# Performance work log

Measured on AMD Instinct MI355X. Metric: run time of the kernel, lower is better.

Reference implementation:

```python
import jax, jax.numpy as jnp
import numpy as np

B, N, D, H, HD, HID, RP_HID = 4, 512, 1024, 16, 64, 4096, 64
EPS = 1e-5


def _ln(h, g, b):
    mu = h.mean(-1, keepdims=True)
    var = h.var(-1, keepdims=True)
    return (h - mu) / jnp.sqrt(var + EPS) * g + b


def setup_inputs() -> dict:
    key = jax.random.key(0)
    ks = jax.random.split(key, 24)
    s = 0.05
    return {
        "x": jax.random.normal(ks[0], (B, N, D), jnp.float32),
        "t_emb": jax.random.normal(ks[1], (B, D), jnp.float32),
        "rel_pos_matrix": jax.random.normal(ks[2], (B, N, N, 2), jnp.float32),
        "agent_mask": jax.random.randint(ks[3], (B, N), 0, 2).astype(jnp.int32),
        # adaLN modulation: Linear(D, 6D)
        "w_ada": jax.random.normal(ks[4], (6 * D, D), jnp.float32) * s,
        "b_ada": jnp.zeros((6 * D,), jnp.float32),
        # LayerNorms
        "g1": jnp.ones((D,), jnp.float32),
        "beta1": jnp.zeros((D,), jnp.float32),
        "g2": jnp.ones((D,), jnp.float32),
        "beta2": jnp.zeros((D,), jnp.float32),
        # attention qkv / proj
        "w_qkv": jax.random.normal(ks[5], (3 * D, D), jnp.float32) * s,
        "b_qkv": jnp.zeros((3 * D,), jnp.float32),
        "w_proj": jax.random.normal(ks[6], (D, D), jnp.float32) * s,
        "b_proj": jnp.zeros((D,), jnp.float32),
        # rel-pos bias MLP: Linear(2,64) -> ReLU -> Linear(64,H)
        "w_rp1": jax.random.normal(ks[7], (RP_HID, 2), jnp.float32) * s,
        "b_rp1": jnp.zeros((RP_HID,), jnp.float32),
        "w_rp2": jax.random.normal(ks[8], (H, RP_HID), jnp.float32) * s,
        "b_rp2": jnp.zeros((H,), jnp.float32),
        # MLP: Linear(D, HID) -> GELU -> Linear(HID, D)
        "w_fc1": jax.random.normal(ks[9], (HID, D), jnp.float32) * s,
        "b_fc1": jnp.zeros((HID,), jnp.float32),
        "w_fc2": jax.random.normal(ks[10], (D, HID), jnp.float32) * s,
        "b_fc2": jnp.zeros((D,), jnp.float32),
    }


def reference(x, t_emb, rel_pos_matrix, agent_mask,
              w_ada, b_ada, g1, beta1, w_qkv, b_qkv, w_proj, b_proj,
              w_rp1, b_rp1, w_rp2, b_rp2, g2, beta2,
              w_fc1, b_fc1, w_fc2, b_fc2):
    b, n, d = x.shape
    # adaLN: SiLU -> Linear -> 6 chunks of [B, D]
    mod = jax.nn.silu(t_emb) @ w_ada.T + b_ada
    shift_s, scale_s, gate_s, shift_m, scale_m, gate_m = jnp.split(mod, 6, axis=1)

    # ---- spatial attention branch ----
    xn = _ln(x, g1, beta1) * (1.0 + scale_s[:, None, :]) + shift_s[:, None, :]
    qkv = (xn @ w_qkv.T + b_qkv).reshape(b, n, 3, H, HD)
    q, k, v = jnp.moveaxis(qkv, 2, 0)  # each [B, N, H, HD]
    attn = jnp.einsum('bnhd,bmhd->bhnm', q, k) * (HD ** -0.5)
    # relative-position bias MLP: [B,N,N,2] -> [B,N,N,H] -> [B,H,N,N]
    bias = jax.nn.relu(rel_pos_matrix @ w_rp1.T + b_rp1) @ w_rp2.T + b_rp2
    attn = attn + bias.transpose(0, 3, 1, 2)
    mask = agent_mask.astype(bool)[:, None, None, :]  # key-side mask [B,1,1,N]
    attn = jnp.where(mask, attn, -jnp.inf)
    p = jax.nn.softmax(attn, axis=-1)
    out = jnp.einsum('bhnm,bmhd->bnhd', p, v).reshape(b, n, d)
    out = out @ w_proj.T + b_proj
    x = x + gate_s[:, None, :] * out

    # ---- gated MLP branch ----
    xn = _ln(x, g2, beta2) * (1.0 + scale_m[:, None, :]) + shift_m[:, None, :]
    h = jax.nn.gelu(xn @ w_fc1.T + b_fc1, approximate=False)
    x = x + gate_m[:, None, :] * (h @ w_fc2.T + b_fc2)
    return x
```

## Files before the change

kernel.cpp:

```cpp
#include <hip/hip_runtime.h>


#define B_ 4
#define N_ 512
#define D_ 1024
#define H_ 16
#define HID_ 4096
#define M_ (B_*N_)

typedef unsigned short u16;
typedef __attribute__((ext_vector_type(8))) short bf16x8;
typedef __attribute__((ext_vector_type(4))) float f32x4;

__device__ __forceinline__ float b2f(u16 u){
  union { unsigned int i; float f; } x; x.i = ((unsigned int)u) << 16; return x.f;
}
__device__ __forceinline__ u16 f2b(float f){
  unsigned int u = __float_as_uint(f);
  return (u16)((u + 0x7fffu + ((u >> 16) & 1u)) >> 16);
}

__device__ __forceinline__ void gload16(const u16* __restrict__ g, u16* l){
#if defined(__has_builtin) && __has_builtin(__builtin_amdgcn_global_load_lds)
  __builtin_amdgcn_global_load_lds(
      (const __attribute__((address_space(1))) unsigned int*)g,
      (__attribute__((address_space(3))) unsigned int*)l, 16, 0, 0);
#else
  *(uint4*)l = *(const uint4*)g;
#endif
}

__global__ __launch_bounds__(256) void k_cvt2(const float* __restrict__ sA, u16* __restrict__ dA,
    int nA, const float* __restrict__ sB, u16* __restrict__ dB){
  int blk = blockIdx.x;
  const float* s; u16* d; size_t i;
  if (blk < nA){ s = sA; d = dA; i = ((size_t)blk*256 + threadIdx.x)*8; }
  else { s = sB; d = dB; i = ((size_t)(blk-nA)*256 + threadIdx.x)*8; }
  float4 a = *(const float4*)(s+i), b = *(const float4*)(s+i+4);
  u16 o[8] = {f2b(a.x),f2b(a.y),f2b(a.z),f2b(a.w),f2b(b.x),f2b(b.y),f2b(b.z),f2b(b.w)};
  *(uint4*)(d+i) = *(const uint4*)o;
}

__global__ __launch_bounds__(256) void k_mod(const float* __restrict__ t_emb,
    const float* __restrict__ w_ada, const float* __restrict__ b_ada,
    float* __restrict__ mod)
{
  __shared__ float st[D_];
  int b = blockIdx.y;
  for (int i = threadIdx.x; i < D_; i += 256){
    float x = t_emb[b*D_ + i];
    st[i] = x / (1.f + __expf(-x));
  }
  __syncthreads();
  int j = blockIdx.x * 256 + threadIdx.x;
  const float* wr = w_ada + (size_t)j * D_;
  float acc = b_ada[j];
  for (int k = 0; k < D_; k += 8){
    float4 p0 = *(const float4*)(wr + k);
    float4 p1 = *(const float4*)(wr + k + 4);
    acc += p0.x*st[k+0] + p0.y*st[k+1] + p0.z*st[k+2] + p0.w*st[k+3];
    acc += p1.x*st[k+4] + p1.y*st[k+5] + p1.z*st[k+6] + p1.w*st[k+7];
  }
  mod[b*6*D_ + j] = acc;
}

__global__ __launch_bounds__(256) void k_lnmod(const float* __restrict__ xin,
    const float* __restrict__ g, const float* __restrict__ be,
    const float* __restrict__ mod, int shift_idx, int scale_idx,
    u16* __restrict__ xn)
{
  int row = blockIdx.x;
  int b = row >> 9;
  float v[4]; float s = 0.f, s2 = 0.f;
  #pragma unroll
  for (int i=0;i<4;i++){
    float x = xin[(size_t)row*D_ + threadIdx.x + i*256];
    v[i] = x; s += x; s2 += x*x;
  }
  #pragma unroll
  for (int o=32;o>0;o>>=1){ s += __shfl_down(s,o); s2 += __shfl_down(s2,o); }
  __shared__ float rs[4], rs2[4];
  int w = threadIdx.x >> 6;
  if ((threadIdx.x & 63)==0){ rs[w]=s; rs2[w]=s2; }
  __syncthreads();
  s = rs[0]+rs[1]+rs[2]+rs[3]; s2 = rs2[0]+rs2[1]+rs2[2]+rs2[3];
  float mu = s * (1.f/D_);
  float var = s2 * (1.f/D_) - mu*mu;
  float rstd = rsqrtf(var + 1e-5f);
  const float* mrow = mod + b*6*D_;
  #pragma unroll
  for (int i=0;i<4;i++){
    int d = threadIdx.x + i*256;
    float xg = (v[i]-mu)*rstd*g[d] + be[d];
    xn[(size_t)row*D_ + d] = f2b(xg * (1.f + mrow[scale_idx*D_ + d]) + mrow[shift_idx*D_ + d]);
  }
}

__global__ __launch_bounds__(256) void k_bias(const float* __restrict__ rel,
    const int* __restrict__ amask,
    const float* __restrict__ w_rp1, const float* __restrict__ b_rp1,
    const float* __restrict__ w_rp2, const float* __restrict__ b_rp2,
    u16* __restrict__ biasbuf)
{
  __shared__ __align__(16) u16 Hs[256*72];
  __shared__ __align__(16) u16 Bs[16*272];
  __shared__ __align__(16) u16 w2s[16*72];
  __shared__ float b2s[16];
  __shared__ u16 msk[256];
  int mh = blockIdx.x, n = blockIdx.y, b = blockIdx.z;
  int tid = threadIdx.x;
  int w = tid >> 6, lane = tid & 63, ln = lane & 15, quad = lane >> 4;

  for (int i = tid; i < 1024; i += 256) w2s[(i>>6)*72 + (i&63)] = f2b(w_rp2[i]);
  if (tid < 16) b2s[tid] = b_rp2[tid];
  msk[tid] = (u16)(amask[b*N_ + mh*256 + tid] != 0);

  {
    float2 r01 = *(const float2*)(rel + ((size_t)((b*N_ + n)*N_) + mh*256 + tid)*2);
    const float* w1 = w_rp1;
    u16 hv[64];
    #pragma unroll
    for (int j=0;j<64;j++){
      float t = w1[2*j]*r01.x + w1[2*j+1]*r01.y + b_rp1[j];
      hv[j] = f2b(t > 0.f ? t : 0.f);
    }
    uint4* dst = (uint4*)&Hs[tid*72];
    #pragma unroll
    for (int c=0;c<8;c++) dst[c] = *(const uint4*)&hv[c*8];
  }
  __syncthreads();

  bf16x8 af0 = *(const bf16x8*)&w2s[ln*72 + quad*8];
  bf16x8 af1 = *(const bf16x8*)&w2s[ln*72 + 32 + quad*8];

  #pragma unroll
  for (int t=0; t<4; t++){
    int mt = w*4 + t;
    bf16x8 bf0 = *(const bf16x8*)&Hs[(mt*16+ln)*72 + quad*8];
    bf16x8 bf1 = *(const bf16x8*)&Hs[(mt*16+ln)*72 + 32 + quad*8];
    f32x4 c = {};
    c = __builtin_amdgcn_mfma_f32_16x16x32_bf16(af0, bf0, c, 0,0,0);
    c = __builtin_amdgcn_mfma_f32_16x16x32_bf16(af1, bf1, c, 0,0,0);
    bool valid = msk[mt*16 + ln] != 0;
    #pragma unroll
    for (int i=0;i<4;i++){
      int h = quad*4 + i;
      float val = valid ? (c[i] + b2s[h]) : -1e30f;
      Bs[h*272 + mt*16 + ln] = f2b(val);
    }
  }
  __syncthreads();

  #pragma unroll
  for (int it=0; it<8; it++){
    int idx = it*256 + tid;
    int r = idx >> 7, cc = idx & 127;
    size_t rb = (((size_t)(b*H_ + r)*N_) + n)*N_ + mh*256;
    ((unsigned int*)(biasbuf + rb))[cc] = ((const unsigned int*)(Bs + r*272))[cc];
  }
}

enum { EPI_FC1=0, EPI_PART=1 };

template<int EPI>
__global__ __launch_bounds__(256) void k_gemm(const u16* __restrict__ A,
    const u16* __restrict__ W, const float* __restrict__ Wb, int K, int Kslice,
    int ldc, u16* __restrict__ part01, u16* __restrict__ part23)
{
  __shared__ __align__(16) u16 Al[128*64];
  __shared__ __align__(16) u16 Wl[128*64];
  int row0 = blockIdx.y*128, col0 = blockIdx.x*128;
  int tid = threadIdx.x;
  int w = tid >> 6, lane = tid & 63, ln = lane & 15, quad = lane >> 4;
  int wy = w >> 1, wx = w & 1;
  int srow = tid >> 3;
  int schunk = (tid & 7) ^ (srow & 7);
  const u16* Ag = A + (size_t)(row0 + srow)*K + schunk*8;
  const u16* Wg = W + (size_t)(col0 + srow)*K + schunk*8;
  int aoff[4][2], woff[4][2];
  #pragma unroll
  for (int ms=0; ms<4; ms++){
    int r = 64*wy + 16*ms + ln;
    #pragma unroll
    for (int kk=0; kk<2; kk++)
      aoff[ms][kk] = r*64 + (((kk*4+quad) ^ (ln&7))*8);
  }
  #pragma unroll
  for (int ns=0; ns<4; ns++){
    int r = 64*wx + 16*ns + ln;
    #pragma unroll
    for (int kk=0; kk<2; kk++)
      woff[ns][kk] = r*64 + (((kk*4+quad) ^ (ln&7))*8);
  }
  f32x4 acc[4][4] = {};
  int kbeg = blockIdx.z * Kslice;
  for (int k0 = kbeg; k0 < kbeg + Kslice; k0 += 64){
    #pragma unroll
    for (int i=0;i<4;i++){
      gload16(Ag + k0 + (size_t)(32*i)*K, Al + i*2048 + tid*8);
      gload16(Wg + k0 + (size_t)(32*i)*K, Wl + i*2048 + tid*8);
    }
    __syncthreads();
    #pragma unroll
    for (int kk=0; kk<2; kk++){
      bf16x8 af[4], bfr[4];
      #pragma unroll
      for (int ms=0; ms<4; ms++) af[ms]  = *(const bf16x8*)&Al[aoff[ms][kk]];
      #pragma unroll
      for (int ns=0; ns<4; ns++) bfr[ns] = *(const bf16x8*)&Wl[woff[ns][kk]];
      #pragma unroll
      for (int ms=0; ms<4; ms++)
        #pragma unroll
        for (int ns=0; ns<4; ns++)
          acc[ms][ns] = __builtin_amdgcn_mfma_f32_16x16x32_bf16(af[ms], bfr[ns], acc[ms][ns], 0,0,0);
    }
    __syncthreads();
  }

  u16* pbase = (EPI == EPI_PART)
             ? ((blockIdx.z < 2 ? part01 : part23) + (size_t)(blockIdx.z & 1)*M_*ldc)
             : part01;
  #pragma unroll
  for (int ms=0; ms<4; ms++){
    #pragma unroll
    for (int ns=0; ns<4; ns++){
      int c = col0 + 64*wx + 16*ns + ln;
      float wb = (EPI == EPI_FC1) ? Wb[c] : 0.f;
      #pragma unroll
      for (int i=0;i<4;i++){
        int r = row0 + 64*wy + 16*ms + quad*4 + i;
        float val = acc[ms][ns][i] + wb;
        if (EPI == EPI_FC1){
          float gl = 0.5f*val*(1.f + erff(val*0.70710678f));
          pbase[(size_t)r*ldc + c] = f2b(gl);
        } else {
          pbase[(size_t)r*ldc + c] = f2b(val);
        }
      }
    }
  }
}

__global__ __launch_bounds__(256) void k_redq(const u16* __restrict__ part,
    const float* __restrict__ Wb, u16* __restrict__ qkvb)
{
  size_t i = ((size_t)blockIdx.x*256 + threadIdx.x)*4;
  int c = (int)(i % 3072);
  uint2 p0 = *(const uint2*)(part + i);
  uint2 p1 = *(const uint2*)(part + (size_t)M_*3072 + i);
  float4 bi = *(const float4*)(Wb + c);
  u16 o[4];
  o[0] = f2b(b2f((u16)(p0.x & 0xffff)) + b2f((u16)(p1.x & 0xffff)) + bi.x);
  o[1] = f2b(b2f((u16)(p0.x >> 16))    + b2f((u16)(p1.x >> 16))    + bi.y);
  o[2] = f2b(b2f((u16)(p0.y & 0xffff)) + b2f((u16)(p1.y & 0xffff)) + bi.z);
  o[3] = f2b(b2f((u16)(p0.y >> 16))    + b2f((u16)(p1.y >> 16))    + bi.w);
  *(uint2*)(qkvb + i) = *(const uint2*)o;
}

template<int GIDX>
__global__ __launch_bounds__(256) void k_red4(const u16* __restrict__ p01,
    const u16* __restrict__ p23, const float* __restrict__ Wb,
    const float* __restrict__ mod, const float* __restrict__ resid,
    float* __restrict__ outp)
{
  size_t i = ((size_t)blockIdx.x*256 + threadIdx.x)*4;
  int c = (int)(i & 1023); int r = (int)(i >> 10); int b = r >> 9;
  uint2 a0 = *(const uint2*)(p01 + i);
  uint2 a1 = *(const uint2*)(p01 + (size_t)M_*D_ + i);
  uint2 a2 = *(const uint2*)(p23 + i);
  uint2 a3 = *(const uint2*)(p23 + (size_t)M_*D_ + i);
  float4 pv;
  pv.x = b2f((u16)(a0.x&0xffff)) + b2f((u16)(a1.x&0xffff)) + b2f((u16)(a2.x&0xffff)) + b2f((u16)(a3.x&0xffff));
  pv.y = b2f((u16)(a0.x>>16))    + b2f((u16)(a1.x>>16))    + b2f((u16)(a2.x>>16))    + b2f((u16)(a3.x>>16));
  pv.z = b2f((u16)(a0.y&0xffff)) + b2f((u16)(a1.y&0xffff)) + b2f((u16)(a2.y&0xffff)) + b2f((u16)(a3.y&0xffff));
  pv.w = b2f((u16)(a0.y>>16))    + b2f((u16)(a1.y>>16))    + b2f((u16)(a2.y>>16))    + b2f((u16)(a3.y>>16));
  float4 x4 = *(const float4*)(resid + i);
  float4 bi = *(const float4*)(Wb + c);
  float4 g4 = *(const float4*)(mod + b*6*D_ + GIDX*D_ + c);
  float4 o;
  o.x = x4.x + g4.x*(pv.x + bi.x);
  o.y = x4.y + g4.y*(pv.y + bi.y);
  o.z = x4.z + g4.z*(pv.z + bi.z);
  o.w = x4.w + g4.w*(pv.w + bi.w);
  *(float4*)(outp + i) = o;
}

__global__ __launch_bounds__(256) void k_attn(const u16* __restrict__ qkv,
    const u16* __restrict__ biasbuf, u16* __restrict__ attn_out)
{
  __shared__ __align__(16) u16 Qs[64*72];
  __shared__ __align__(16) u16 Ks[64*72];
  __shared__ __align__(16) u16 Vt[64*72];
  __shared__ __align__(16) u16 Ps[4*16*72];
  int nt = blockIdx.x, h = blockIdx.y, b = blockIdx.z;
  int n0 = nt*64;
  int tid = threadIdx.x;
  int w = tid >> 6, lane = tid & 63, ln = lane & 15, quad = lane >> 4;

  {
    int row = tid >> 2, cb = (tid & 3)*16;
    const u16* src = qkv + (size_t)(b*N_ + n0 + row)*3072 + h*64 + cb;
    uint4 q0 = *(const uint4*)src, q1 = *(const uint4*)(src+8);
    uint4* dst = (uint4*)&Qs[row*72 + cb];
    dst[0] = q0; dst[1] = q1;
  }
  __syncthreads();
  bf16x8 qf[2];
  qf[0] = *(const bf16x8*)&Qs[(16*w+ln)*72 + quad*8];
  qf[1] = *(const bf16x8*)&Qs[(16*w+ln)*72 + 32 + quad*8];

  f32x4 oacc[4] = {};
  float rmax[4] = {-3e38f,-3e38f,-3e38f,-3e38f};
  float rsum[4] = {0.f,0.f,0.f,0.f};
  const u16* bp = biasbuf + (((size_t)(b*H_ + h)*N_) + n0 + 16*w)*N_ + ln;

  for (int mt = 0; mt < 8; mt++){
    __syncthreads();
    {
      int r = tid >> 2, cb = (tid & 3)*16;
      const u16* kp = qkv + (size_t)(b*N_ + mt*64 + r)*3072 + 1024 + h*64 + cb;
      uint4 k0 = *(const uint4*)kp, k1 = *(const uint4*)(kp+8);
      uint4* kd = (uint4*)&Ks[r*72 + cb];
      kd[0] = k0; kd[1] = k1;
      const u16* vp = qkv + (size_t)(b*N_ + mt*64 + r)*3072 + 2048 + h*64 + cb;
      uint4 v0 = *(const uint4*)vp, v1 = *(const uint4*)(vp+8);
      u16 ve[16];
      *(uint4*)&ve[0] = v0; *(uint4*)&ve[8] = v1;
      #pragma unroll
      for (int j=0;j<16;j++) Vt[(cb+j)*72 + r] = ve[j];
    }
    __syncthreads();

    u16 bl[4][4];
    #pragma unroll
    for (int cs=0; cs<4; cs++)
      #pragma unroll
      for (int i=0;i<4;i++)
        bl[cs][i] = bp[(size_t)(quad*4+i)*N_ + mt*64 + 16*cs];

    f32x4 s[4];
    #pragma unroll
    for (int cs=0; cs<4; cs++){
      bf16x8 k0f = *(const bf16x8*)&Ks[(16*cs+ln)*72 + quad*8];
      bf16x8 k1f = *(const bf16x8*)&Ks[(16*cs+ln)*72 + 32 + quad*8];
      f32x4 z = {};
      z = __builtin_amdgcn_mfma_f32_16x16x32_bf16(qf[0], k0f, z, 0,0,0);
      z = __builtin_amdgcn_mfma_f32_16x16x32_bf16(qf[1], k1f, z, 0,0,0);
      s[cs] = z;
    }
    #pragma unroll
    for (int cs=0; cs<4; cs++)
      #pragma unroll
      for (int i=0;i<4;i++)
        s[cs][i] = s[cs][i]*0.125f + b2f(bl[cs][i]);

    #pragma unroll
    for (int i=0;i<4;i++){
      float tm = fmaxf(fmaxf(s[0][i], s[1][i]), fmaxf(s[2][i], s[3][i]));
      #pragma unroll
      for (int o=1;o<16;o<<=1) tm = fmaxf(tm, __shfl_xor(tm, o));
      float nm = fmaxf(rmax[i], tm);
      float alpha = __expf(rmax[i] - nm);
      rmax[i] = nm;
      float ps = 0.f;
      #pragma unroll
      for (int cs=0; cs<4; cs++){
        float p = __expf(s[cs][i] - nm);
        s[cs][i] = p; ps += p;
      }
      #pragma unroll
      for (int o=1;o<16;o<<=1) ps += __shfl_xor(ps, o);
      rsum[i] = rsum[i]*alpha + ps;
      #pragma unroll
      for (int ds=0; ds<4; ds++) oacc[ds][i] *= alpha;
    }

    #pragma unroll
    for (int cs=0; cs<4; cs++)
      #pragma unroll
      for (int i=0;i<4;i++)
        Ps[w*1152 + (quad*4+i)*72 + 16*cs + ln] = f2b(s[cs][i]);

    bf16x8 pf0 = *(const bf16x8*)&Ps[w*1152 + ln*72 + quad*8];
    bf16x8 pf1 = *(const bf16x8*)&Ps[w*1152 + ln*72 + 32 + quad*8];
    #pragma unroll
    for (int ds=0; ds<4; ds++){
      bf16x8 v0f = *(const bf16x8*)&Vt[(16*ds+ln)*72 + quad*8];
      bf16x8 v1f = *(const bf16x8*)&Vt[(16*ds+ln)*72 + 32 + quad*8];
      oacc[ds] = __builtin_amdgcn_mfma_f32_16x16x32_bf16(pf0, v0f, oacc[ds], 0,0,0);
      oacc[ds] = __builtin_amdgcn_mfma_f32_16x16x32_bf16(pf1, v1f, oacc[ds], 0,0,0);
    }
  }

  #pragma unroll
  for (int i=0;i<4;i++){
    float inv = 1.f / rsum[i];
    int r = b*N_ + n0 + 16*w + quad*4 + i;
    #pragma unroll
    for (int ds=0; ds<4; ds++)
      attn_out[(size_t)r*D_ + h*64 + 16*ds + ln] = f2b(oacc[ds][i]*inv);
  }
}

extern "C" void kernel_launch(void* const* d_in, const int* in_sizes, int n_in,
                              void* d_out, int out_size, void* d_ws, size_t ws_size,
                              hipStream_t stream) {
  const float* x      = (const float*)d_in[0];
  const float* t_emb  = (const float*)d_in[1];
  const float* rel    = (const float*)d_in[2];
  const int*   amask  = (const int*)d_in[3];
  const float* w_ada  = (const float*)d_in[4];
  const float* b_ada  = (const float*)d_in[5];
  const float* g1     = (const float*)d_in[6];
  const float* beta1  = (const float*)d_in[7];
  const float* g2     = (const float*)d_in[8];
  const float* beta2  = (const float*)d_in[9];
  const float* w_qkv  = (const float*)d_in[10];
  const float* b_qkv  = (const float*)d_in[11];
  const float* w_proj = (const float*)d_in[12];
  const float* b_proj = (const float*)d_in[13];
  const float* w_rp1  = (const float*)d_in[14];
  const float* b_rp1  = (const float*)d_in[15];
  const float* w_rp2  = (const float*)d_in[16];
  const float* b_rp2  = (const float*)d_in[17];
  const float* w_fc1  = (const float*)d_in[18];
  const float* b_fc1  = (const float*)d_in[19];
  const float* w_fc2  = (const float*)d_in[20];
  const float* b_fc2  = (const float*)d_in[21];
  float* outp = (float*)d_out;

  const size_t MB = 1u<<20;
  char* wsb = (char*)d_ws;
  float* mod   = (float*)(wsb);
  u16*  xn     = (u16*) (wsb + 131072);
  float* xm    = (float*)(wsb + 131072 + 4*MB);
  u16*  wqkvb  = (u16*) (wsb + 131072 + 12*MB);
  u16*  wprojb = (u16*) (wsb + 131072 + 18*MB);
  u16*  partb  = (u16*) (wsb + 131072 + 20*MB);
  char*  S     = wsb + 131072 + 28*MB;
  u16*  qkvb   = (u16*)(S);
  u16*  qkvpart= (u16*)(S + 12*MB);
  u16*  biasb  = (u16*)(S + 12*MB);
  u16*  projp23= (u16*)(S);
  u16*  hb     = (u16*)(S);
  u16*  wfc1b  = (u16*)(S + 16*MB);
  u16*  wfc2b  = (u16*)(S + 24*MB);
  u16*  fc2p23 = (u16*)(S + 32*MB);

  k_cvt2<<<2048, 256, 0, stream>>>(w_qkv, wqkvb, 1536, w_proj, wprojb);
  k_mod<<<dim3(6*D_/256, B_), 256, 0, stream>>>(t_emb, w_ada, b_ada, mod);
  k_lnmod<<<M_, 256, 0, stream>>>(x, g1, beta1, mod, 0, 1, xn);
  k_gemm<EPI_PART><<<dim3(3072/128, M_/128, 2), 256, 0, stream>>>(
      xn, wqkvb, nullptr, D_, D_/2, 3072, qkvpart, qkvpart);
  k_redq<<<6144, 256, 0, stream>>>(qkvpart, b_qkv, qkvb);
  k_bias<<<dim3(2, N_, B_), 256, 0, stream>>>(rel, amask, w_rp1, b_rp1, w_rp2, b_rp2, biasb);
  k_attn<<<dim3(8, H_, B_), 256, 0, stream>>>(qkvb, biasb, xn);
  k_cvt2<<<4096, 256, 0, stream>>>(w_fc1, wfc1b, 2048, w_fc2, wfc2b);
  k_gemm<EPI_PART><<<dim3(D_/128, M_/128, 4), 256, 0, stream>>>(
      xn, wprojb, nullptr, D_, D_/4, D_, partb, projp23);
  k_red4<2><<<2048, 256, 0, stream>>>(partb, projp23, b_proj, mod, x, xm);
  k_lnmod<<<M_, 256, 0, stream>>>(xm, g2, beta2, mod, 3, 4, xn);
  k_gemm<EPI_FC1><<<dim3(HID_/128, M_/128), 256, 0, stream>>>(
      xn, wfc1b, b_fc1, D_, D_, HID_, hb, nullptr);
  k_gemm<EPI_PART><<<dim3(D_/128, M_/128, 4), 256, 0, stream>>>(
      hb, wfc2b, nullptr, HID_, HID_/4, D_, partb, fc2p23);
  k_red4<5><<<2048, 256, 0, stream>>>(partb, fc2p23, b_fc2, mod, xm, outp);
}
```

Before: 369.5 us.

## Replace split-K QKV with 64-row GEMM tile and fuse proj reduction with LayerNorm

Adds a 64x128-tile GEMM kernel with a fused bias (and optional GELU) epilogue. It is used for the QKV projection, which removes the split-K partial writes and the separate reduction kernel, and for FC1, which doubles the number of blocks. The proj-output reduction and residual update are fused with the second LayerNorm-modulation into one row kernel, removing one kernel and one read of the fp32 residual. The trade-off is a smaller tile with less reuse per block in exchange for more blocks and fewer passes over memory.

Result: faster. 356.9 us (-3.4%).

```diff
diff --git a/kernel.cpp b/kernel.cpp
--- a/kernel.cpp
+++ b/kernel.cpp
@@ -160,11 +160,80 @@
   }
 }
 
-enum { EPI_FC1=0, EPI_PART=1 };
+enum { EPI_PLAIN=0, EPI_GELU=1 };
 
 template<int EPI>
+__global__ __launch_bounds__(256) void k_gemm64(const u16* __restrict__ A,
+    const u16* __restrict__ W, const float* __restrict__ Wb, int K, int ldc,
+    u16* __restrict__ o_u16)
+{
+  __shared__ __align__(16) u16 Al[64*64];
+  __shared__ __align__(16) u16 Wl[128*64];
+  int row0 = blockIdx.y*64, col0 = blockIdx.x*128;
+  int tid = threadIdx.x;
+  int w = tid >> 6, lane = tid & 63, ln = lane & 15, quad = lane >> 4;
+  int wy = w >> 1, wx = w & 1;
+  int srow = tid >> 3;
+  int schunk = (tid & 7) ^ (srow & 7);
+  const u16* Ag = A + (size_t)(row0 + srow)*K + schunk*8;
+  const u16* Wg = W + (size_t)(col0 + srow)*K + schunk*8;
+  int aoff[2][2], woff[4][2];
+  #pragma unroll
+  for (int ms=0; ms<2; ms++){
+    int r = 32*wy + 16*ms + ln;
+    #pragma unroll
+    for (int kk=0; kk<2; kk++)
+      aoff[ms][kk] = r*64 + (((kk*4+quad) ^ (ln&7))*8);
+  }
+  #pragma unroll
+  for (int ns=0; ns<4; ns++){
+    int r = 64*wx + 16*ns + ln;
+    #pragma unroll
+    for (int kk=0; kk<2; kk++)
+      woff[ns][kk] = r*64 + (((kk*4+quad) ^ (ln&7))*8);
+  }
+  f32x4 acc[2][4] = {};
+  for (int k0 = 0; k0 < K; k0 += 64){
+    gload16(Ag + k0,                  Al + tid*8);
+    gload16(Ag + k0 + (size_t)32*K,   Al + 2048 + tid*8);
+    #pragma unroll
+    for (int i=0;i<4;i++)
+      gload16(Wg + k0 + (size_t)(32*i)*K, Wl + i*2048 + tid*8);
+    __syncthreads();
+    #pragma unroll
+    for (int kk=0; kk<2; kk++){
+      bf16x8 af[2], bfr[4];
+      #pragma unroll
+      for (int ms=0; ms<2; ms++) af[ms]  = *(const bf16x8*)&Al[aoff[ms][kk]];
+      #pragma unroll
+      for (int ns=0; ns<4; ns++) bfr[ns] = *(const bf16x8*)&Wl[woff[ns][kk]];
+      #pragma unroll
+      for (int ms=0; ms<2; ms++)
+        #pragma unroll
+        for (int ns=0; ns<4; ns++)
+          acc[ms][ns] = __builtin_amdgcn_mfma_f32_16x16x32_bf16(af[ms], bfr[ns], acc[ms][ns], 0,0,0);
+    }
+    __syncthreads();
+  }
+  #pragma unroll
+  for (int ms=0; ms<2; ms++){
+    #pragma unroll
+    for (int ns=0; ns<4; ns++){
+      int c = col0 + 64*wx + 16*ns + ln;
+      float wb = Wb[c];
+      #pragma unroll
+      for (int i=0;i<4;i++){
+        int r = row0 + 32*wy + 16*ms + quad*4 + i;
+        float val = acc[ms][ns][i] + wb;
+        if (EPI == EPI_GELU) val = 0.5f*val*(1.f + erff(val*0.70710678f));
+        o_u16[(size_t)r*ldc + c] = f2b(val);
+      }
+    }
+  }
+}
+
 __global__ __launch_bounds__(256) void k_gemm(const u16* __restrict__ A,
-    const u16* __restrict__ W, const float* __restrict__ Wb, int K, int Kslice,
+    const u16* __restrict__ W, int K, int Kslice,
     int ldc, u16* __restrict__ part01, u16* __restrict__ part23)
 {
   __shared__ __align__(16) u16 Al[128*64];
@@ -216,45 +285,19 @@
     }
     __syncthreads();
   }
-
-  u16* pbase = (EPI == EPI_PART)
-             ? ((blockIdx.z < 2 ? part01 : part23) + (size_t)(blockIdx.z & 1)*M_*ldc)
-             : part01;
+  u16* pbase = (blockIdx.z < 2 ? part01 : part23) + (size_t)(blockIdx.z & 1)*M_*ldc;
   #pragma unroll
   for (int ms=0; ms<4; ms++){
     #pragma unroll
     for (int ns=0; ns<4; ns++){
       int c = col0 + 64*wx + 16*ns + ln;
-      float wb = (EPI == EPI_FC1) ? Wb[c] : 0.f;
       #pragma unroll
       for (int i=0;i<4;i++){
         int r = row0 + 64*wy + 16*ms + quad*4 + i;
-        float val = acc[ms][ns][i] + wb;
-        if (EPI == EPI_FC1){
-          float gl = 0.5f*val*(1.f + erff(val*0.70710678f));
-          pbase[(size_t)r*ldc + c] = f2b(gl);
-        } else {
-          pbase[(size_t)r*ldc + c] = f2b(val);
-        }
+        pbase[(size_t)r*ldc + c] = f2b(acc[ms][ns][i]);
       }
     }
   }
-}
-
-__global__ __launch_bounds__(256) void k_redq(const u16* __restrict__ part,
-    const float* __restrict__ Wb, u16* __restrict__ qkvb)
-{
-  size_t i = ((size_t)blockIdx.x*256 + threadIdx.x)*4;
-  int c = (int)(i % 3072);
-  uint2 p0 = *(const uint2*)(part + i);
-  uint2 p1 = *(const uint2*)(part + (size_t)M_*3072 + i);
-  float4 bi = *(const float4*)(Wb + c);
-  u16 o[4];
-  o[0] = f2b(b2f((u16)(p0.x & 0xffff)) + b2f((u16)(p1.x & 0xffff)) + bi.x);
-  o[1] = f2b(b2f((u16)(p0.x >> 16))    + b2f((u16)(p1.x >> 16))    + bi.y);
-  o[2] = f2b(b2f((u16)(p0.y & 0xffff)) + b2f((u16)(p1.y & 0xffff)) + bi.z);
-  o[3] = f2b(b2f((u16)(p0.y >> 16))    + b2f((u16)(p1.y >> 16))    + bi.w);
-  *(uint2*)(qkvb + i) = *(const uint2*)o;
 }
 
 template<int GIDX>
@@ -283,6 +326,58 @@
   o.z = x4.z + g4.z*(pv.z + bi.z);
   o.w = x4.w + g4.w*(pv.w + bi.w);
   *(float4*)(outp + i) = o;
+}
+
+__global__ __launch_bounds__(256) void k_redln(const u16* __restrict__ p01,
+    const u16* __restrict__ p23, const float* __restrict__ Wb,
+    const float* __restrict__ mod, const float* __restrict__ resid,
+    const float* __restrict__ g, const float* __restrict__ be,
+    float* __restrict__ xm, u16* __restrict__ xn)
+{
+  int row = blockIdx.x, b = row >> 9, tid = threadIdx.x;
+  size_t i = (size_t)row*D_ + tid*4;
+  int c = tid*4;
+  uint2 a0 = *(const uint2*)(p01 + i);
+  uint2 a1 = *(const uint2*)(p01 + (size_t)M_*D_ + i);
+  uint2 a2 = *(const uint2*)(p23 + i);
+  uint2 a3 = *(const uint2*)(p23 + (size_t)M_*D_ + i);
+  float4 pv;
+  pv.x = b2f((u16)(a0.x&0xffff)) + b2f((u16)(a1.x&0xffff)) + b2f((u16)(a2.x&0xffff)) + b2f((u16)(a3.x&0xffff));
+  pv.y = b2f((u16)(a0.x>>16))    + b2f((u16)(a1.x>>16))    + b2f((u16)(a2.x>>16))    + b2f((u16)(a3.x>>16));
+  pv.z = b2f((u16)(a0.y&0xffff)) + b2f((u16)(a1.y&0xffff)) + b2f((u16)(a2.y&0xffff)) + b2f((u16)(a3.y&0xffff));
+  pv.w = b2f((u16)(a0.y>>16))    + b2f((u16)(a1.y>>16))    + b2f((u16)(a2.y>>16))    + b2f((u16)(a3.y>>16));
+  float4 x4 = *(const float4*)(resid + i);
+  float4 bi = *(const float4*)(Wb + c);
+  float4 g4 = *(const float4*)(mod + b*6*D_ + 2*D_ + c);
+  float4 mid;
+  mid.x = x4.x + g4.x*(pv.x + bi.x);
+  mid.y = x4.y + g4.y*(pv.y + bi.y);
+  mid.z = x4.z + g4.z*(pv.z + bi.z);
+  mid.w = x4.w + g4.w*(pv.w + bi.w);
+  *(float4*)(xm + i) = mid;
+  float s = mid.x+mid.y+mid.z+mid.w;
+  float s2 = mid.x*mid.x+mid.y*mid.y+mid.z*mid.z+mid.w*mid.w;
+  #pragma unroll
+  for (int o=32;o>0;o>>=1){ s += __shfl_down(s,o); s2 += __shfl_down(s2,o); }
+  __shared__ float rs[4], rs2[4];
+  int w = tid >> 6;
+  if ((tid & 63)==0){ rs[w]=s; rs2[w]=s2; }
+  __syncthreads();
+  s = rs[0]+rs[1]+rs[2]+rs[3]; s2 = rs2[0]+rs2[1]+rs2[2]+rs2[3];
+  float mu = s * (1.f/D_);
+  float var = s2 * (1.f/D_) - mu*mu;
+  float rstd = rsqrtf(var + 1e-5f);
+  const float* mrow = mod + b*6*D_;
+  float4 gg = *(const float4*)(g + c);
+  float4 bb = *(const float4*)(be + c);
+  float4 sc = *(const float4*)(mrow + 4*D_ + c);
+  float4 sh = *(const float4*)(mrow + 3*D_ + c);
+  u16 o[4];
+  o[0] = f2b(((mid.x-mu)*rstd*gg.x + bb.x)*(1.f+sc.x) + sh.x);
+  o[1] = f2b(((mid.y-mu)*rstd*gg.y + bb.y)*(1.f+sc.y) + sh.y);
+  o[2] = f2b(((mid.z-mu)*rstd*gg.z + bb.z)*(1.f+sc.z) + sh.z);
+  o[3] = f2b(((mid.w-mu)*rstd*gg.w + bb.w)*(1.f+sc.w) + sh.w);
+  *(uint2*)(xn + i) = *(const uint2*)o;
 }
 
 __global__ __launch_bounds__(256) void k_attn(const u16* __restrict__ qkv,
@@ -439,7 +534,6 @@
   u16*  partb  = (u16*) (wsb + 131072 + 20*MB);
   char*  S     = wsb + 131072 + 28*MB;
   u16*  qkvb   = (u16*)(S);
-  u16*  qkvpart= (u16*)(S + 12*MB);
   u16*  biasb  = (u16*)(S + 12*MB);
   u16*  projp23= (u16*)(S);
   u16*  hb     = (u16*)(S);
@@ -450,19 +544,17 @@
   k_cvt2<<<2048, 256, 0, stream>>>(w_qkv, wqkvb, 1536, w_proj, wprojb);
   k_mod<<<dim3(6*D_/256, B_), 256, 0, stream>>>(t_emb, w_ada, b_ada, mod);
   k_lnmod<<<M_, 256, 0, stream>>>(x, g1, beta1, mod, 0, 1, xn);
-  k_gemm<EPI_PART><<<dim3(3072/128, M_/128, 2), 256, 0, stream>>>(
-      xn, wqkvb, nullptr, D_, D_/2, 3072, qkvpart, qkvpart);
-  k_redq<<<6144, 256, 0, stream>>>(qkvpart, b_qkv, qkvb);
+  k_gemm64<EPI_PLAIN><<<dim3(3072/128, M_/64), 256, 0, stream>>>(
+      xn, wqkvb, b_qkv, D_, 3072, qkvb);
   k_bias<<<dim3(2, N_, B_), 256, 0, stream>>>(rel, amask, w_rp1, b_rp1, w_rp2, b_rp2, biasb);
   k_attn<<<dim3(8, H_, B_), 256, 0, stream>>>(qkvb, biasb, xn);
   k_cvt2<<<4096, 256, 0, stream>>>(w_fc1, wfc1b, 2048, w_fc2, wfc2b);
-  k_gemm<EPI_PART><<<dim3(D_/128, M_/128, 4), 256, 0, stream>>>(
-      xn, wprojb, nullptr, D_, D_/4, D_, partb, projp23);
-  k_red4<2><<<2048, 256, 0, stream>>>(partb, projp23, b_proj, mod, x, xm);
-  k_lnmod<<<M_, 256, 0, stream>>>(xm, g2, beta2, mod, 3, 4, xn);
-  k_gemm<EPI_FC1><<<dim3(HID_/128, M_/128), 256, 0, stream>>>(
-      xn, wfc1b, b_fc1, D_, D_, HID_, hb, nullptr);
-  k_gemm<EPI_PART><<<dim3(D_/128, M_/128, 4), 256, 0, stream>>>(
-      hb, wfc2b, nullptr, HID_, HID_/4, D_, partb, fc2p23);
+  k_gemm<<<dim3(D_/128, M_/128, 4), 256, 0, stream>>>(
+      xn, wprojb, D_, D_/4, D_, partb, projp23);
+  k_redln<<<M_, 256, 0, stream>>>(partb, projp23, b_proj, mod, x, g2, beta2, xm, xn);
+  k_gemm64<EPI_GELU><<<dim3(HID_/128, M_/64), 256, 0, stream>>>(
+      xn, wfc1b, b_fc1, D_, HID_, hb);
+  k_gemm<<<dim3(D_/128, M_/128, 4), 256, 0, stream>>>(
+      hb, wfc2b, HID_, HID_/4, D_, partb, fc2p23);
   k_red4<5><<<2048, 256, 0, stream>>>(partb, fc2p23, b_fc2, mod, xm, outp);
 }
```
